# Kernel optimization log

Measured on AMD Instinct MI355X. Metric: run time of the kernel, lower is better.

The kernel has to match this reference:

```python
import jax, jax.numpy as jnp
import numpy as np

MSA_DIM = 256
PAIR_DIM = 128
HEAD_DIM = 32


def setup_inputs() -> dict:
    key = jax.random.key(0)
    ks = jax.random.split(key, 9)
    n_seq, seq_len = 128, 256
    s = lambda d: 1.0 / np.sqrt(d)
    return {
        "msa_input": jax.random.normal(ks[0], (n_seq, seq_len, MSA_DIM), jnp.float32),
        "norm_w": jnp.ones((MSA_DIM,), jnp.float32),
        "norm_b": jnp.zeros((MSA_DIM,), jnp.float32),
        "w1": jax.random.normal(ks[1], (MSA_DIM, HEAD_DIM), jnp.float32) * s(MSA_DIM),
        "b1": jax.random.normal(ks[2], (HEAD_DIM,), jnp.float32) * 0.01,
        "w2": jax.random.normal(ks[3], (MSA_DIM, HEAD_DIM), jnp.float32) * s(MSA_DIM),
        "b2": jax.random.normal(ks[4], (HEAD_DIM,), jnp.float32) * 0.01,
        "w3": jax.random.normal(ks[5], (HEAD_DIM * HEAD_DIM, PAIR_DIM), jnp.float32) * s(HEAD_DIM * HEAD_DIM),
        "b3": jax.random.normal(ks[6], (PAIR_DIM,), jnp.float32) * 0.01,
    }


def _layernorm(x, w, b, eps=1e-5):
    mu = jnp.mean(x, axis=-1, keepdims=True)
    var = jnp.mean(jnp.square(x - mu), axis=-1, keepdims=True)
    return (x - mu) * jax.lax.rsqrt(var + eps) * w + b


def reference(msa_input, norm_w, norm_b, w1, b1, w2, b2, w3, b3):
    n_seq, seq_len, _ = msa_input.shape
    normed = _layernorm(msa_input, norm_w, norm_b)
    # proj_a uses linear2, proj_b uses linear1 (as in the torch code)
    proj_a = normed @ w2 + b2  # [n, i, c]
    proj_b = normed @ w1 + b1  # [n, j, c]
    # mean over MSA depth n expressed as a GEMM-style contraction
    outer = jnp.einsum('nia,njb->ijab', proj_a, proj_b) / n_seq  # [i, j, c, c]
    outer = outer.reshape(seq_len, seq_len, -1)
    return outer @ w3 + b3  # [i, j, pair_dim]
```

## Files before the change

kernel.cpp:

```cpp
#include <hip/hip_runtime.h>
#include <hip/hip_bf16.h>
#include <stdint.h>

#define SEQ  256
#define PD   128

typedef short bf16x8 __attribute__((ext_vector_type(8)));
typedef float f32x4  __attribute__((ext_vector_type(4)));
typedef float f32x16 __attribute__((ext_vector_type(16)));
typedef short s16x4  __attribute__((ext_vector_type(4)));

__device__ __forceinline__ short f2bf(float x) {
    union { float f; uint32_t u; } v; v.f = x;
    uint32_t r = v.u + 0x7FFFu + ((v.u >> 16) & 1u);
    return (short)(r >> 16);
}

__device__ __forceinline__ void gld16(const void* g, void* l) {
    __builtin_amdgcn_global_load_lds(
        (const __attribute__((address_space(1))) void*)g,
        (__attribute__((address_space(3))) void*)l, 16, 0, 0);
}

__global__ __launch_bounds__(256) void k_prep(const float* __restrict__ w1,
                                              const float* __restrict__ w2,
                                              const float* __restrict__ w3,
                                              short* __restrict__ w12t,
                                              short* __restrict__ w3p) {
    int id = blockIdx.x * 256 + threadIdx.x;
    if (id < 2048) {
        int col = id >> 5, cp = id & 31;
        int c = cp ^ (col & 7);
        bf16x8 o;
        #pragma unroll
        for (int e = 0; e < 8; ++e) {
            int k = c * 8 + e;
            float v = (col < 32) ? w2[k * 32 + col] : w1[k * 32 + (col - 32)];
            o[e] = f2bf(v);
        }
        *(bf16x8*)(w12t + id * 8) = o;
    } else {
        int id2 = id - 2048;
        int pg = id2 >> 12, ks = (id2 >> 6) & 63, l2 = id2 & 63;
        bf16x8 o;
        #pragma unroll
        for (int e = 0; e < 8; ++e) {
            int k = ks * 16 + (l2 >> 5) * 8 + e;
            int p = pg * 32 + (l2 & 31);
            o[e] = f2bf(w3[k * 128 + p]);
        }
        *(bf16x8*)(w3p + id2 * 8) = o;
    }
}

__global__ __launch_bounds__(256) void k_fused(const float* __restrict__ msa,
                                               const float* __restrict__ nw,
                                               const float* __restrict__ nb_,
                                               const float* __restrict__ b1,
                                               const float* __restrict__ b2,
                                               const short* __restrict__ w12t,
                                               short* __restrict__ pa,
                                               short* __restrict__ pb) {
    __shared__ short smem[32768];
    int i = blockIdx.x, nbk = blockIdx.y;
    int t = threadIdx.x, l = t & 63, w = t >> 6;

    #pragma unroll
    for (int it = 0; it < 8; ++it) {
        int ci = it * 256 + t;
        gld16(w12t + (size_t)ci * 8, smem + (it * 256 + (t & ~63)) * 8);
    }
    float4 x[16];
    const float* basep = msa + ((size_t)(nbk * 64 + w * 16) * SEQ + i) * 256 + l * 4;
    #pragma unroll
    for (int j = 0; j < 16; ++j)
        x[j] = *(const float4*)(basep + (size_t)j * SEQ * 256);
    float4 wv = *(const float4*)(nw + l * 4);
    float4 bv = *(const float4*)(nb_ + l * 4);
    #pragma unroll
    for (int j = 0; j < 16; ++j) {
        float s = x[j].x + x[j].y + x[j].z + x[j].w;
        #pragma unroll
        for (int o = 32; o > 0; o >>= 1) s += __shfl_xor(s, o, 64);
        float mu = s * (1.0f / 256.0f);
        float dx = x[j].x - mu, dy = x[j].y - mu, dz = x[j].z - mu, dw = x[j].w - mu;
        float sq = dx * dx + dy * dy + dz * dz + dw * dw;
        #pragma unroll
        for (int o = 32; o > 0; o >>= 1) sq += __shfl_xor(sq, o, 64);
        float rs = rsqrtf(sq * (1.0f / 256.0f) + 1e-5f);
        s16x4 o4;
        o4[0] = f2bf(dx * rs * wv.x + bv.x);
        o4[1] = f2bf(dy * rs * wv.y + bv.y);
        o4[2] = f2bf(dz * rs * wv.z + bv.z);
        o4[3] = f2bf(dw * rs * wv.w + bv.w);
        int row = w * 16 + j;
        *(s16x4*)((char*)smem + 32768 + row * 512 + (((l >> 1) ^ (row & 7)) * 16) + (l & 1) * 8) = o4;
    }
    __syncthreads();
    int lr = l & 15, lk = l >> 4;
    f32x4 acc[4] = {};
    #pragma unroll
    for (int ks = 0; ks < 8; ++ks) {
        int c = ks * 4 + lk;
        int xr = w * 16 + lr;
        bf16x8 xf = *(bf16x8*)((char*)smem + 32768 + xr * 512 + ((c ^ (xr & 7)) * 16));
        #pragma unroll
        for (int af = 0; af < 4; ++af) {
            int rw = af * 16 + lr;
            bf16x8 wf = *(bf16x8*)((char*)smem + rw * 512 + ((c ^ (rw & 7)) * 16));
            acc[af] = __builtin_amdgcn_mfma_f32_16x16x32_bf16(wf, xf, acc[af], 0, 0, 0);
        }
    }
    int nglob = nbk * 64 + w * 16 + lr;
    #pragma unroll
    for (int af = 0; af < 4; ++af) {
        #pragma unroll
        for (int r = 0; r < 4; ++r) {
            int cc = af * 16 + lk * 4 + r;
            float bias = (cc < 32) ? b2[cc] : b1[cc - 32];
            short v = f2bf(acc[af][r] + bias);
            if (cc < 32) pa[(size_t)(i * 32 + cc) * 128 + nglob] = v;
            else         pb[(size_t)(i * 32 + (cc - 32)) * 128 + nglob] = v;
        }
    }
}

__global__ __launch_bounds__(1024) void k_outer(const short* __restrict__ pa,
                                                const short* __restrict__ pb,
                                                const short* __restrict__ w3p,
                                                const float* __restrict__ b3,
                                                float* __restrict__ out) {
    __shared__ short smem[65536];
    int t = threadIdx.x, l = t & 63, w = t >> 6;
    int lin = blockIdx.x;
    int swz = (lin & 7) * 128 + (lin >> 3);
    int bi = swz >> 5, bj = swz & 31;

    const short* srcA = pa + (size_t)bi * 256 * 128;
    const short* srcB = pb + (size_t)bj * 256 * 128;
    #pragma unroll
    for (int it = 0; it < 8; ++it) {
        int half = it >> 2, sub = it & 3;
        int buf = sub >> 1;
        int row = (sub & 1) * 128 + (t >> 3);
        int c1  = t & 7;
        int gch = (c1 ^ (row & 7)) + half * 8;
        const short* g = (buf ? srcB : srcA) + (size_t)row * 128 + gch * 8;
        int row0 = (sub & 1) * 128 + ((t & ~63) >> 3);
        gld16(g, smem + half * 32768 + buf * 16384 + row0 * 64);
    }
    asm volatile("s_waitcnt vmcnt(4)" ::: "memory");
    __builtin_amdgcn_sched_barrier(0);
    __builtin_amdgcn_s_barrier();
    __builtin_amdgcn_sched_barrier(0);

    int wm = w & 3, wn = w >> 2;
    int l31 = l & 31, lh = l >> 5;
    f32x16 acc1[2][2] = {};
    #pragma unroll
    for (int ks2 = 0; ks2 < 4; ++ks2) {
        int g = ks2 * 2 + lh, half = g >> 3, c = g & 7;
        bf16x8 af[2], bfr[2];
        #pragma unroll
        for (int fm = 0; fm < 2; ++fm) {
            int row = wm * 64 + fm * 32 + l31;
            af[fm] = *(bf16x8*)(smem + half * 32768 + row * 64 + (c ^ (row & 7)) * 8);
        }
        #pragma unroll
        for (int fn = 0; fn < 2; ++fn) {
            int row = wn * 64 + fn * 32 + l31;
            bfr[fn] = *(bf16x8*)(smem + half * 32768 + 16384 + row * 64 + (c ^ (row & 7)) * 8);
        }
        __builtin_amdgcn_s_setprio(1);
        #pragma unroll
        for (int fn = 0; fn < 2; ++fn)
            #pragma unroll
            for (int fm = 0; fm < 2; ++fm)
                acc1[fn][fm] = __builtin_amdgcn_mfma_f32_32x32x16_bf16(bfr[fn], af[fm], acc1[fn][fm], 0, 0, 0);
        __builtin_amdgcn_s_setprio(0);
    }
    __syncthreads();
    #pragma unroll
    for (int ks2 = 4; ks2 < 8; ++ks2) {
        int g = ks2 * 2 + lh, half = g >> 3, c = g & 7;
        bf16x8 af[2], bfr[2];
        #pragma unroll
        for (int fm = 0; fm < 2; ++fm) {
            int row = wm * 64 + fm * 32 + l31;
            af[fm] = *(bf16x8*)(smem + half * 32768 + row * 64 + (c ^ (row & 7)) * 8);
        }
        #pragma unroll
        for (int fn = 0; fn < 2; ++fn) {
            int row = wn * 64 + fn * 32 + l31;
            bfr[fn] = *(bf16x8*)(smem + half * 32768 + 16384 + row * 64 + (c ^ (row & 7)) * 8);
        }
        __builtin_amdgcn_s_setprio(1);
        #pragma unroll
        for (int fn = 0; fn < 2; ++fn)
            #pragma unroll
            for (int fm = 0; fm < 2; ++fm)
                acc1[fn][fm] = __builtin_amdgcn_mfma_f32_32x32x16_bf16(bfr[fn], af[fm], acc1[fn][fm], 0, 0, 0);
        __builtin_amdgcn_s_setprio(0);
    }
    __syncthreads();

    const float inv_n = 1.0f / 128.0f;
    #pragma unroll
    for (int fn = 0; fn < 2; ++fn) {
        #pragma unroll
        for (int fm = 0; fm < 2; ++fm) {
            int pair = (wm * 2 + fm) * 8 + wn * 2 + fn;
            #pragma unroll
            for (int g = 0; g < 4; ++g) {
                int q  = l31 * 4 + g;
                int qp = q ^ (pair & 7) ^ ((q >> 3) & 7);
                s16x4 o;
                #pragma unroll
                for (int j = 0; j < 4; ++j) o[j] = f2bf(acc1[fn][fm][g * 4 + j] * inv_n);
                *(s16x4*)(smem + pair * 1024 + qp * 8 + lh * 4) = o;
            }
        }
    }
    __syncthreads();

    int pg = w & 3, kh = w >> 2;
    f32x16 acc2[2] = {};
    __builtin_amdgcn_s_setprio(1);
    #pragma unroll
    for (int ksi = 0; ksi < 16; ++ksi) {
        int ksg = kh * 16 + ksi;
        bf16x8 b2f = *(const bf16x8*)(w3p + ((size_t)(pg * 64 + ksg) * 64 + l) * 8);
        int qr  = ksg * 2 + lh;
        int sig = (ksg >> 2) & 7;
        #pragma unroll
        for (int mq = 0; mq < 2; ++mq) {
            int prow = mq * 32 + l31;
            int qp = qr ^ (prow & 7) ^ sig;
            bf16x8 a2 = *(bf16x8*)(smem + prow * 1024 + qp * 8);
            acc2[mq] = __builtin_amdgcn_mfma_f32_32x32x16_bf16(a2, b2f, acc2[mq], 0, 0, 0);
        }
    }
    __builtin_amdgcn_s_setprio(0);
    __syncthreads();

    float* scratch = (float*)smem;
    if (kh != 0) {
        int base = ((kh - 1) * 4 + pg) * 2;
        #pragma unroll
        for (int mq = 0; mq < 2; ++mq)
            #pragma unroll
            for (int r = 0; r < 16; ++r)
                scratch[((base + mq) * 16 + r) * 64 + l] = acc2[mq][r];
    }
    __syncthreads();
    if (kh == 0) {
        int p = pg * 32 + l31;
        float bias = b3[p];
        #pragma unroll
        for (int mq = 0; mq < 2; ++mq) {
            #pragma unroll
            for (int r = 0; r < 16; ++r) {
                float v = acc2[mq][r];
                #pragma unroll
                for (int kk = 0; kk < 3; ++kk)
                    v += scratch[(((kk * 4 + pg) * 2 + mq) * 16 + r) * 64 + l];
                int pair = mq * 32 + (r & 3) + 8 * (r >> 2) + 4 * lh;
                int oi = bi * 8 + (pair >> 3), oj = bj * 8 + (pair & 7);
                out[((size_t)(oi * 256 + oj)) * 128 + p] = v + bias;
            }
        }
    }
}

extern "C" void kernel_launch(void* const* d_in, const int* in_sizes, int n_in,
                              void* d_out, int out_size, void* d_ws, size_t ws_size,
                              hipStream_t stream) {
    const float* msa = (const float*)d_in[0];
    const float* nw  = (const float*)d_in[1];
    const float* nbv = (const float*)d_in[2];
    const float* w1  = (const float*)d_in[3];
    const float* b1  = (const float*)d_in[4];
    const float* w2  = (const float*)d_in[5];
    const float* b2  = (const float*)d_in[6];
    const float* w3  = (const float*)d_in[7];
    const float* b3  = (const float*)d_in[8];
    float* out = (float*)d_out;

    char* ws = (char*)d_ws;
    short* pa   = (short*)ws;
    short* pb   = (short*)(ws + (2u << 20));
    short* w3p  = (short*)(ws + (4u << 20));
    short* w12t = (short*)(ws + (4u << 20) + (256u << 10));

    k_prep <<<72, 256, 0, stream>>>(w1, w2, w3, w12t, w3p);
    k_fused<<<dim3(256, 2), 256, 0, stream>>>(msa, nw, nbv, b1, b2, w12t, pa, pb);
    k_outer<<<1024, 1024, 0, stream>>>(pa, pb, w3p, b3, out);
}
```

Before: 144.8 us.

## Double-buffer LDS fragments, prefetch W3 into registers, fold 1/n into W3

The outer-product GEMM loop now double-buffers its LDS fragment loads, so the next k-step's reads are issued before the current MFMAs. W3 fragments for the second GEMM are prefetched from global memory into registers, half before the bf16 conversion and half after the barrier, which hides their load latency. The 1/n scaling moves into W3 preprocessing, and the bf16 pack uses the hardware v_cvt_pk_bf16_f32 instead of manual rounding. The cost is higher register pressure (16 extra bf16x8 fragments), which could reduce occupancy or cause spills. Folding 1/128 into W3 before bf16 rounding is exact in value, but the larger unscaled intermediate is now rounded to bf16.

```diff
diff --git a/kernel.cpp b/kernel.cpp
--- a/kernel.cpp
+++ b/kernel.cpp
@@ -47,7 +47,7 @@
         for (int e = 0; e < 8; ++e) {
             int k = ks * 16 + (l2 >> 5) * 8 + e;
             int p = pg * 32 + (l2 & 31);
-            o[e] = f2bf(w3[k * 128 + p]);
+            o[e] = f2bf(w3[k * 128 + p] * 0.0078125f);
         }
         *(bf16x8*)(w3p + id2 * 8) = o;
     }
@@ -157,10 +157,9 @@
     int wm = w & 3, wn = w >> 2;
     int l31 = l & 31, lh = l >> 5;
     f32x16 acc1[2][2] = {};
-    #pragma unroll
-    for (int ks2 = 0; ks2 < 4; ++ks2) {
+
+    auto loadf = [&](int ks2, bf16x8* af, bf16x8* bfr) {
         int g = ks2 * 2 + lh, half = g >> 3, c = g & 7;
-        bf16x8 af[2], bfr[2];
         #pragma unroll
         for (int fm = 0; fm < 2; ++fm) {
             int row = wm * 64 + fm * 32 + l31;
@@ -171,40 +170,45 @@
             int row = wn * 64 + fn * 32 + l31;
             bfr[fn] = *(bf16x8*)(smem + half * 32768 + 16384 + row * 64 + (c ^ (row & 7)) * 8);
         }
+    };
+
+    bf16x8 fra[2][2], frb[2][2];
+    loadf(0, fra[0], frb[0]);
+    #pragma unroll
+    for (int ks2 = 0; ks2 < 4; ++ks2) {
+        if (ks2 < 3) loadf(ks2 + 1, fra[(ks2 + 1) & 1], frb[(ks2 + 1) & 1]);
         __builtin_amdgcn_s_setprio(1);
         #pragma unroll
         for (int fn = 0; fn < 2; ++fn)
             #pragma unroll
             for (int fm = 0; fm < 2; ++fm)
-                acc1[fn][fm] = __builtin_amdgcn_mfma_f32_32x32x16_bf16(bfr[fn], af[fm], acc1[fn][fm], 0, 0, 0);
+                acc1[fn][fm] = __builtin_amdgcn_mfma_f32_32x32x16_bf16(
+                    frb[ks2 & 1][fn], fra[ks2 & 1][fm], acc1[fn][fm], 0, 0, 0);
         __builtin_amdgcn_s_setprio(0);
     }
     __syncthreads();
+    loadf(4, fra[0], frb[0]);
     #pragma unroll
     for (int ks2 = 4; ks2 < 8; ++ks2) {
-        int g = ks2 * 2 + lh, half = g >> 3, c = g & 7;
-        bf16x8 af[2], bfr[2];
-        #pragma unroll
-        for (int fm = 0; fm < 2; ++fm) {
-            int row = wm * 64 + fm * 32 + l31;
-            af[fm] = *(bf16x8*)(smem + half * 32768 + row * 64 + (c ^ (row & 7)) * 8);
-        }
-        #pragma unroll
-        for (int fn = 0; fn < 2; ++fn) {
-            int row = wn * 64 + fn * 32 + l31;
-            bfr[fn] = *(bf16x8*)(smem + half * 32768 + 16384 + row * 64 + (c ^ (row & 7)) * 8);
-        }
+        if (ks2 < 7) loadf(ks2 + 1, fra[(ks2 + 1) & 1], frb[(ks2 + 1) & 1]);
         __builtin_amdgcn_s_setprio(1);
         #pragma unroll
         for (int fn = 0; fn < 2; ++fn)
             #pragma unroll
             for (int fm = 0; fm < 2; ++fm)
-                acc1[fn][fm] = __builtin_amdgcn_mfma_f32_32x32x16_bf16(bfr[fn], af[fm], acc1[fn][fm], 0, 0, 0);
+                acc1[fn][fm] = __builtin_amdgcn_mfma_f32_32x32x16_bf16(
+                    frb[ks2 & 1][fn], fra[ks2 & 1][fm], acc1[fn][fm], 0, 0, 0);
         __builtin_amdgcn_s_setprio(0);
     }
     __syncthreads();
 
-    const float inv_n = 1.0f / 128.0f;
+    int pg = w & 3, kh = w >> 2;
+    const short* wbase = w3p + ((size_t)(pg * 64 + kh * 16) * 64 + l) * 8;
+    bf16x8 b2f[16];
+    #pragma unroll
+    for (int ksi = 0; ksi < 8; ++ksi)
+        b2f[ksi] = *(const bf16x8*)(wbase + ksi * 512);
+
     #pragma unroll
     for (int fn = 0; fn < 2; ++fn) {
         #pragma unroll
@@ -214,22 +218,28 @@
             for (int g = 0; g < 4; ++g) {
                 int q  = l31 * 4 + g;
                 int qp = q ^ (pair & 7) ^ ((q >> 3) & 7);
-                s16x4 o;
-                #pragma unroll
-                for (int j = 0; j < 4; ++j) o[j] = f2bf(acc1[fn][fm][g * 4 + j] * inv_n);
-                *(s16x4*)(smem + pair * 1024 + qp * 8 + lh * 4) = o;
+                union { uint32_t u[2]; s16x4 v; } pk;
+                asm("v_cvt_pk_bf16_f32 %0, %1, %2"
+                    : "=v"(pk.u[0])
+                    : "v"(acc1[fn][fm][g * 4 + 0]), "v"(acc1[fn][fm][g * 4 + 1]));
+                asm("v_cvt_pk_bf16_f32 %0, %1, %2"
+                    : "=v"(pk.u[1])
+                    : "v"(acc1[fn][fm][g * 4 + 2]), "v"(acc1[fn][fm][g * 4 + 3]));
+                *(s16x4*)(smem + pair * 1024 + qp * 8 + lh * 4) = pk.v;
             }
         }
     }
     __syncthreads();
 
-    int pg = w & 3, kh = w >> 2;
+    #pragma unroll
+    for (int ksi = 8; ksi < 16; ++ksi)
+        b2f[ksi] = *(const bf16x8*)(wbase + ksi * 512);
+
     f32x16 acc2[2] = {};
     __builtin_amdgcn_s_setprio(1);
     #pragma unroll
     for (int ksi = 0; ksi < 16; ++ksi) {
         int ksg = kh * 16 + ksi;
-        bf16x8 b2f = *(const bf16x8*)(w3p + ((size_t)(pg * 64 + ksg) * 64 + l) * 8);
         int qr  = ksg * 2 + lh;
         int sig = (ksg >> 2) & 7;
         #pragma unroll
@@ -237,7 +247,7 @@
             int prow = mq * 32 + l31;
             int qp = qr ^ (prow & 7) ^ sig;
             bf16x8 a2 = *(bf16x8*)(smem + prow * 1024 + qp * 8);
-            acc2[mq] = __builtin_amdgcn_mfma_f32_32x32x16_bf16(a2, b2f, acc2[mq], 0, 0, 0);
+            acc2[mq] = __builtin_amdgcn_mfma_f32_32x32x16_bf16(a2, b2f[ksi], acc2[mq], 0, 0, 0);
         }
     }
     __builtin_amdgcn_s_setprio(0);
```

Result: faster. 141.8 us (-2.1%).
